# Optimization experiments

Hardware: AMD Instinct MI355X
Metric: run time of the kernel (lower is better)

Reference implementation:

```python
import jax, jax.numpy as jnp
import numpy as np

# Module dims (match init_kwargs)
D_IN = 1024
N_PRI = 2048
D_PRI = 16
N_CLS = 25
D_CLS = 16
ITERS = 3
B = 64
EPS = 1e-6


def layer_norm(x, g, b, eps=1e-5):
    m = x.mean(-1, keepdims=True)
    v = ((x - m) ** 2).mean(-1, keepdims=True)
    return (x - m) / jnp.sqrt(v + eps) * g + b


def setup_inputs() -> dict:
    key = jax.random.key(0)
    ks = jax.random.split(key, 6)
    s = lambda n: 1.0 / np.sqrt(n)
    return {
        "z": jax.random.normal(ks[0], (B, D_IN), jnp.float32),
        # to_primary: Linear(d_in, n_primary*d_primary)
        "w1": jax.random.normal(ks[1], (D_IN, N_PRI * D_PRI), jnp.float32) * s(D_IN),
        "b1": jnp.zeros((N_PRI * D_PRI,), jnp.float32),
        # primary_act: LayerNorm(d_in) -> Linear(d_in, n_primary) -> Sigmoid
        "ln1_g": jnp.ones((D_IN,), jnp.float32),
        "ln1_b": jnp.zeros((D_IN,), jnp.float32),
        "w2": jax.random.normal(ks[2], (D_IN, N_PRI), jnp.float32) * s(D_IN),
        "b2": jnp.zeros((N_PRI,), jnp.float32),
        # CapsuleFC transform + EM routing params
        "w_caps": jax.random.normal(ks[3], (N_PRI, D_PRI, N_CLS, D_CLS), jnp.float32) * s(D_PRI),
        "beta_u": jnp.zeros((N_CLS,), jnp.float32),
        "beta_a": jnp.zeros((N_CLS,), jnp.float32),
        # to_logits: LayerNorm(d_class) -> Linear(d_class, 1)
        "ln2_g": jnp.ones((D_CLS,), jnp.float32),
        "ln2_b": jnp.zeros((D_CLS,), jnp.float32),
        "w3": jax.random.normal(ks[4], (D_CLS, 1), jnp.float32) * s(D_CLS),
        "b3": jnp.zeros((1,), jnp.float32),
    }


def em_routing(V, a_in, beta_u, beta_a, n_iter):
    # V: (b, n_in, n_out, d) votes; a_in: (b, n_in) primary activations
    b, n, o, d = V.shape
    R = jnp.full((b, n, o), 1.0 / o, V.dtype)  # routing assignments
    lam = jnp.asarray(1.0, V.dtype)            # inverse temperature
    for _ in range(n_iter):
        # M-step: weighted mean/variance per output capsule
        r = R * a_in[:, :, None]                                  # (b,n,o)
        r_sum = r.sum(axis=1) + EPS                               # (b,o)
        mu = jnp.einsum('bno,bnod->bod', r, V) / r_sum[..., None]  # (b,o,d)
        diff2 = (V - mu[:, None]) ** 2                            # (b,n,o,d)
        sigma2 = jnp.einsum('bno,bnod->bod', r, diff2) / r_sum[..., None] + EPS
        cost = (beta_u[None, :, None] + 0.5 * jnp.log(sigma2)) * r_sum[..., None]
        a_out = jax.nn.sigmoid(lam * (beta_a[None, :] - cost.sum(-1)))  # (b,o)
        # E-step: Gaussian log-likelihood of each vote under each output capsule
        logp = (-0.5 * (diff2 / sigma2[:, None]).sum(-1)
                - 0.5 * jnp.log(sigma2).sum(-1)[:, None, :])      # (b,n,o)
        R = jax.nn.softmax(jnp.log(a_out + EPS)[:, None, :] + logp, axis=-1)
    return mu, a_out, R


def reference(z, w1, b1, ln1_g, ln1_b, w2, b2, w_caps, beta_u, beta_a,
              ln2_g, ln2_b, w3, b3):
    b = z.shape[0]
    # primary poses (no squash: use_squash_primary=False)
    primary_pose = (z @ w1 + b1).reshape(b, N_PRI, D_PRI)
    # primary activations
    primary_act = jnp.clip(jax.nn.sigmoid(layer_norm(z, ln1_g, ln1_b) @ w2 + b2), 0.0, 1.0)
    # votes: each primary capsule predicts each class capsule's pose
    V = jnp.einsum('bni,niod->bnod', primary_pose, w_caps)  # (B, N_PRI, N_CLS, D_CLS)
    class_pose, class_act, q = em_routing(V, primary_act, beta_u, beta_a, ITERS)
    logits = (layer_norm(class_pose, ln2_g, ln2_b) @ w3 + b3).squeeze(-1)  # (B, N_CLS)
    acts = jnp.linalg.norm(class_pose, axis=-1)                            # (B, N_CLS)
    return logits, acts, class_pose, q
```

## Files before the change

kernel.cpp:

```cpp
#include <hip/hip_runtime.h>
#include <hip/hip_bf16.h>
#include <cstdio>

#define B     64
#define DIN   1024
#define NPRI  2048
#define DPRI  16
#define NCLS  25
#define DCLS  16
#define EMEPS 1e-6f
#define LNEPS 1e-5f
#define KS2   8
#define NCH   32

#define OFF_POSE 0
#define OFF_ZN   (OFF_POSE + NPRI*DPRI*B)
#define OFF_ACTT (OFF_ZN + B*DIN)
#define OFF_G2P  (OFF_ACTT + NPRI*B)
#define OFF_V    (OFF_G2P + KS2*NPRI*B)
#define V_FLOATS (NPRI*NCLS*B*DCLS/2)
#define OFF_R    (OFF_V + V_FLOATS)
#define R_FLOATS (NPRI*NCLS*B/2)
#define OFF_PART (OFF_R + R_FLOATS)
#define OFF_MU   (OFF_PART + NCLS*NCH*33*B)
#define OFF_MI4  (OFF_MU + NCLS*DCLS*B)
#define OFF_BASE (OFF_MI4 + NCLS*8*B*4)
#define OFF_ZH   (OFF_BASE + NCLS*B)
#define WS_FLOATS (OFF_ZH + B*DIN/2)

typedef __attribute__((ext_vector_type(8))) _Float16 f16x8;
typedef __attribute__((ext_vector_type(4))) float f32x4;

__device__ __forceinline__ unsigned pack_f16(float a, float b) {
  union { _Float16 h[2]; unsigned u; } x;
  x.h[0] = (_Float16)a; x.h[1] = (_Float16)b;
  return x.u;
}
__device__ __forceinline__ float f16lo(unsigned u) {
  union { unsigned u; _Float16 h[2]; } x; x.u = u; return (float)x.h[0];
}
__device__ __forceinline__ float f16hi(unsigned u) {
  union { unsigned u; _Float16 h[2]; } x; x.u = u; return (float)x.h[1];
}
__device__ __forceinline__ unsigned short f16bits(float a) {
  union { _Float16 h; unsigned short u; } x; x.h = (_Float16)a; return x.u;
}
__device__ __forceinline__ float f16val(unsigned short u) {
  union { unsigned short u; _Float16 h; } x; x.u = u; return (float)x.h;
}

__global__ __launch_bounds__(256) void k_lnzh(const float* __restrict__ z,
                                              const float* __restrict__ g,
                                              const float* __restrict__ bb,
                                              float* __restrict__ zn,
                                              unsigned* __restrict__ zh) {
  int row = blockIdx.x, t = threadIdx.x;
  const float* zr = z + row * DIN;
  float4 v = ((const float4*)zr)[t];
  uint2 hz = {pack_f16(v.x, v.y), pack_f16(v.z, v.w)};
  *(uint2*)&zh[row * 512 + t * 2] = hz;
  float s  = v.x + v.y + v.z + v.w;
  float s2 = v.x*v.x + v.y*v.y + v.z*v.z + v.w*v.w;
  for (int off = 32; off; off >>= 1) {
    s  += __shfl_down(s, off);
    s2 += __shfl_down(s2, off);
  }
  __shared__ float ls[8];
  int wv = t >> 6, ln = t & 63;
  if (ln == 0) { ls[wv*2] = s; ls[wv*2+1] = s2; }
  __syncthreads();
  s  = ls[0] + ls[2] + ls[4] + ls[6];
  s2 = ls[1] + ls[3] + ls[5] + ls[7];
  float mean = s * (1.0f / DIN);
  float var  = s2 * (1.0f / DIN) - mean * mean;
  float inv  = 1.0f / sqrtf(var + LNEPS);
  float4 gg = ((const float4*)g)[t];
  float4 bv = ((const float4*)bb)[t];
  float4 o;
  o.x = (v.x - mean) * inv * gg.x + bv.x;
  o.y = (v.y - mean) * inv * gg.y + bv.y;
  o.z = (v.z - mean) * inv * gg.z + bv.z;
  o.w = (v.w - mean) * inv * gg.w + bv.w;
  ((float4*)(zn + row * DIN))[t] = o;
}

__global__ __launch_bounds__(512) void k_gemm1m(const unsigned* __restrict__ zh,
                                                const float* __restrict__ w1,
                                                const float* __restrict__ b1,
                                                float* __restrict__ poseT) {
  __shared__ __align__(16) unsigned bt[2][64 * 68];
  __shared__ __align__(16) unsigned zl[2][64 * 68];
  int t = threadIdx.x;
  int c0 = blockIdx.x * 64;
  int l = t & 63, w = t >> 6;
  int kh = w >> 2, cw = w & 3;
  int c15 = l & 15, kq = l >> 4;
  int h  = t >> 8;
  int th = t & 255;
  int s_kp = th >> 2;
  int s_q  = th & 3;

  f32x4 acc0 = {0,0,0,0}, acc1 = {0,0,0,0}, acc2 = {0,0,0,0}, acc3 = {0,0,0,0};

  float4 wr0[4], wr1[4];
  uint4  zr4[4];
  {
    int k0 = h * 512;
#pragma unroll
    for (int u = 0; u < 4; ++u) {
      int cq = s_q + 4 * u;
      const float* src0 = w1 + (size_t)(k0 + 2 * s_kp) * 32768 + c0 + cq * 4;
      wr0[u] = *(const float4*)src0;
      wr1[u] = *(const float4*)(src0 + 32768);
      zr4[u] = *(const uint4*)&zh[(size_t)s_kp * 512 + (k0 >> 1) + cq * 4];
    }
  }

  for (int it = 0; it < 4; ++it) {
#pragma unroll
    for (int u = 0; u < 4; ++u) {
      int cq = s_q + 4 * u;
      unsigned* dst = &bt[h][(cq * 4) * 68 + s_kp];
      dst[0]   = pack_f16(wr0[u].x, wr1[u].x);
      dst[68]  = pack_f16(wr0[u].y, wr1[u].y);
      dst[136] = pack_f16(wr0[u].z, wr1[u].z);
      dst[204] = pack_f16(wr0[u].w, wr1[u].w);
      *(uint4*)&zl[h][s_kp * 68 + cq * 4] = zr4[u];
    }
    __syncthreads();
    if (it < 3) {
      int k0n = (h * 4 + it + 1) * 128;
#pragma unroll
      for (int u = 0; u < 4; ++u) {
        int cq = s_q + 4 * u;
        const float* src0 = w1 + (size_t)(k0n + 2 * s_kp) * 32768 + c0 + cq * 4;
        wr0[u] = *(const float4*)src0;
        wr1[u] = *(const float4*)(src0 + 32768);
        zr4[u] = *(const uint4*)&zh[(size_t)s_kp * 512 + (k0n >> 1) + cq * 4];
      }
    }
#pragma unroll
    for (int ks = 0; ks < 4; ++ks) {
      union { uint4 u; f16x8 hh; } bf, a0, a1, a2, a3;
      bf.u = *(const uint4*)&bt[kh][(cw * 16 + c15) * 68 + ks * 16 + kq * 4];
      a0.u = *(const uint4*)&zl[kh][(c15)      * 68 + ks * 16 + kq * 4];
      a1.u = *(const uint4*)&zl[kh][(16 + c15) * 68 + ks * 16 + kq * 4];
      a2.u = *(const uint4*)&zl[kh][(32 + c15) * 68 + ks * 16 + kq * 4];
      a3.u = *(const uint4*)&zl[kh][(48 + c15) * 68 + ks * 16 + kq * 4];
      acc0 = __builtin_amdgcn_mfma_f32_16x16x32_f16(a0.hh, bf.hh, acc0, 0, 0, 0);
      acc1 = __builtin_amdgcn_mfma_f32_16x16x32_f16(a1.hh, bf.hh, acc1, 0, 0, 0);
      acc2 = __builtin_amdgcn_mfma_f32_16x16x32_f16(a2.hh, bf.hh, acc2, 0, 0, 0);
      acc3 = __builtin_amdgcn_mfma_f32_16x16x32_f16(a3.hh, bf.hh, acc3, 0, 0, 0);
    }
    __syncthreads();
  }

  float* red = (float*)&zl[0][0];
  if (kh == 1) {
    int cc = cw * 16 + c15;
    *(float4*)&red[cc * 68 + kq * 4]      = *(float4*)&acc0;
    *(float4*)&red[cc * 68 + 16 + kq * 4] = *(float4*)&acc1;
    *(float4*)&red[cc * 68 + 32 + kq * 4] = *(float4*)&acc2;
    *(float4*)&red[cc * 68 + 48 + kq * 4] = *(float4*)&acc3;
  }
  __syncthreads();
  if (kh == 0) {
    int cc = cw * 16 + c15;
    int c = c0 + cc;
    float bc = b1[c];
    float4 r0 = *(float4*)&red[cc * 68 + kq * 4];
    float4 r1 = *(float4*)&red[cc * 68 + 16 + kq * 4];
    float4 r2 = *(float4*)&red[cc * 68 + 32 + kq * 4];
    float4 r3 = *(float4*)&red[cc * 68 + 48 + kq * 4];
    float* pdst = poseT + (size_t)c * 64 + kq * 4;
    float4 o0 = {acc0[0] + r0.x + bc, acc0[1] + r0.y + bc, acc0[2] + r0.z + bc, acc0[3] + r0.w + bc};
    float4 o1 = {acc1[0] + r1.x + bc, acc1[1] + r1.y + bc, acc1[2] + r1.z + bc, acc1[3] + r1.w + bc};
    float4 o2 = {acc2[0] + r2.x + bc, acc2[1] + r2.y + bc, acc2[2] + r2.z + bc, acc2[3] + r2.w + bc};
    float4 o3 = {acc3[0] + r3.x + bc, acc3[1] + r3.y + bc, acc3[2] + r3.z + bc, acc3[3] + r3.w + bc};
    *(float4*)&pdst[0]  = o0;
    *(float4*)&pdst[16] = o1;
    *(float4*)&pdst[32] = o2;
    *(float4*)&pdst[48] = o3;
  }
}

__global__ __launch_bounds__(256, 2) void k_gemm2p(const float* __restrict__ zn,
                                                   const float* __restrict__ w2,
                                                   float* __restrict__ part) {
  __shared__ __align__(16) float znT[128 * 68];
  __shared__ __align__(16) float wl[128 * 68];
  int t = threadIdx.x;
  int c0 = blockIdx.x * 64;
  int k0 = blockIdx.y * 128;
  int zr_ = t >> 2, za = t & 3;
  int wk = t >> 1, wc = (t & 1) * 32;

#pragma unroll
  for (int jj = 0; jj < 4; ++jj) {
    int kb = za * 8 + jj * 32;
    const float* src = zn + zr_ * DIN + k0 + kb;
    float4 v0 = *(const float4*)src;
    float4 v1 = *(const float4*)(src + 4);
    znT[(kb+0)*68 + zr_] = v0.x; znT[(kb+1)*68 + zr_] = v0.y;
    znT[(kb+2)*68 + zr_] = v0.z; znT[(kb+3)*68 + zr_] = v0.w;
    znT[(kb+4)*68 + zr_] = v1.x; znT[(kb+5)*68 + zr_] = v1.y;
    znT[(kb+6)*68 + zr_] = v1.z; znT[(kb+7)*68 + zr_] = v1.w;
  }
  const float* wsrc = w2 + (size_t)(k0 + wk) * NPRI + c0 + wc;
#pragma unroll
  for (int j = 0; j < 8; ++j)
    *(float4*)&wl[wk * 68 + wc + j * 4] = *(const float4*)(wsrc + j * 4);
  __syncthreads();

  int r0 = (t >> 4) * 4, c0l = (t & 15) * 4;
  float acc[4][4];
#pragma unroll
  for (int j = 0; j < 4; ++j)
#pragma unroll
    for (int i = 0; i < 4; ++i) acc[j][i] = 0.f;

#pragma unroll 4
  for (int k = 0; k < 128; ++k) {
    float4 z4 = *(const float4*)&znT[k * 68 + r0];
    float4 w4 = *(const float4*)&wl[k * 68 + c0l];
    float zz[4] = {z4.x, z4.y, z4.z, z4.w};
    float ww[4] = {w4.x, w4.y, w4.z, w4.w};
#pragma unroll
    for (int j = 0; j < 4; ++j)
#pragma unroll
      for (int i = 0; i < 4; ++i) acc[j][i] += ww[j] * zz[i];
  }
  float* pdst = part + ((size_t)blockIdx.y * NPRI + c0 + c0l) * 64 + r0;
#pragma unroll
  for (int j = 0; j < 4; ++j) {
    float4 o = {acc[j][0], acc[j][1], acc[j][2], acc[j][3]};
    *(float4*)&pdst[j * 64] = o;
  }
}

__global__ __launch_bounds__(256) void k_gemm2r(const float* __restrict__ part,
                                                const float* __restrict__ b2,
                                                float* __restrict__ actt) {
  int idx = blockIdx.x * 256 + threadIdx.x;
  float4 s = {0.f, 0.f, 0.f, 0.f};
#pragma unroll
  for (int kz = 0; kz < KS2; ++kz) {
    float4 v = *(const float4*)&part[(size_t)kz * NPRI * 64 + idx * 4];
    s.x += v.x; s.y += v.y; s.z += v.z; s.w += v.w;
  }
  int c = (idx * 4) >> 6;
  float bc = b2[c];
  float4 o;
  o.x = fminf(fmaxf(1.0f / (1.0f + expf(-(s.x + bc))), 0.0f), 1.0f);
  o.y = fminf(fmaxf(1.0f / (1.0f + expf(-(s.y + bc))), 0.0f), 1.0f);
  o.z = fminf(fmaxf(1.0f / (1.0f + expf(-(s.z + bc))), 0.0f), 1.0f);
  o.w = fminf(fmaxf(1.0f / (1.0f + expf(-(s.w + bc))), 0.0f), 1.0f);
  *(float4*)&actt[idx * 4] = o;
}

__global__ __launch_bounds__(256) void k_votes(const float* __restrict__ poseT,
                                               const float* __restrict__ wcaps,
                                               unsigned* __restrict__ V) {
  __shared__ __align__(16) float wl[6400];
  __shared__ __align__(16) float pl[64 * 16];
  int n = blockIdx.x, t = threadIdx.x;
  const float* wsrc = wcaps + (size_t)n * 6400;
  for (int idx = t * 4; idx < 6400; idx += 1024)
    *(float4*)(wl + idx) = *(const float4*)(wsrc + idx);
  {
    float4 v = *(const float4*)(poseT + n * 1024 + t * 4);
    int i = (t * 4) >> 6, b = (t * 4) & 63;
    pl[(b+0)*16 + i] = v.x; pl[(b+1)*16 + i] = v.y;
    pl[(b+2)*16 + i] = v.z; pl[(b+3)*16 + i] = v.w;
  }
  __syncthreads();
  if (t >= 200) return;
  int o = t / 8, d0 = (t % 8) * 2;
  float w0[16], w1_[16];
#pragma unroll
  for (int i = 0; i < 16; ++i) {
    w0[i]  = wl[(i * 25 + o) * 16 + d0];
    w1_[i] = wl[(i * 25 + o) * 16 + d0 + 1];
  }
  unsigned* vd = V + (((size_t)n * 25 + o) * 64 * 16 + d0) / 2;
  for (int b = 0; b < 64; ++b) {
    const float* pb = &pl[b * 16];
    float a0 = 0.f, a1 = 0.f;
#pragma unroll
    for (int i = 0; i < 16; ++i) {
      float p = pb[i];
      a0 += p * w0[i];
      a1 += p * w1_[i];
    }
    vd[b * 8] = pack_f16(a0, a1);
  }
}

template <bool UNIFORM>
__global__ __launch_bounds__(256) void k_stats(const unsigned* __restrict__ V,
                                               const float* __restrict__ actt,
                                               const unsigned short* __restrict__ Rh,
                                               float* __restrict__ part) {
  int o = blockIdx.y;
  int t = threadIdx.x, b = t & 63, wv = t >> 6;
  float S0 = 0.f, S1[16], S2[16];
#pragma unroll
  for (int d = 0; d < 16; ++d) { S1[d] = 0.f; S2[d] = 0.f; }
  int n0 = blockIdx.x * 64 + wv * 16;
#pragma unroll 2
  for (int k = 0; k < 16; ++k) {
    int n = n0 + k;
    float a = actt[n * 64 + b];
    float r = UNIFORM ? a * (1.0f / 25.0f)
                      : f16val(Rh[((size_t)n * 25 + o) * 64 + b]) * a;
    const uint4* vp = (const uint4*)(V + (((size_t)n * 25 + o) * 64 + b) * 8);
    uint4 u0 = vp[0], u1 = vp[1];
    unsigned uu[8] = {u0.x, u0.y, u0.z, u0.w, u1.x, u1.y, u1.z, u1.w};
    S0 += r;
#pragma unroll
    for (int q = 0; q < 8; ++q) {
      float v0 = f16lo(uu[q]), v1 = f16hi(uu[q]);
      float t0 = r * v0, t1 = r * v1;
      S1[2*q]   += t0;          S1[2*q+1] += t1;
      S2[2*q]   += t0 * v0;     S2[2*q+1] += t1 * v1;
    }
  }
  __shared__ float red[4 * 33 * 64];
  red[(wv * 33 + 0) * 64 + b] = S0;
#pragma unroll
  for (int d = 0; d < 16; ++d) {
    red[(wv * 33 + 1 + d) * 64 + b]  = S1[d];
    red[(wv * 33 + 17 + d) * 64 + b] = S2[d];
  }
  __syncthreads();
  if (wv == 0) {
    for (int s = 0; s < 33; ++s) {
      float tot = red[s * 64 + b] + red[(33 + s) * 64 + b] +
                  red[(66 + s) * 64 + b] + red[(99 + s) * 64 + b];
      part[((o * NCH + blockIdx.x) * 33 + s) * 64 + b] = tot;
    }
  }
}

template <bool FINAL>
__global__ __launch_bounds__(256) void k_redfin(const float* __restrict__ part,
                                                const float* __restrict__ beta_u,
                                                const float* __restrict__ beta_a,
                                                float* __restrict__ mu,
                                                float* __restrict__ mi4,
                                                float* __restrict__ basew,
                                                const float* __restrict__ g2,
                                                const float* __restrict__ bb2,
                                                const float* __restrict__ w3,
                                                const float* __restrict__ b3,
                                                float* __restrict__ out) {
  __shared__ float st[33 * 64];
  int o = blockIdx.x, t = threadIdx.x;
  for (int slot = t; slot < 33 * 64; slot += 256) {
    float s = 0.f;
    const float* pp = part + (size_t)o * NCH * 2112 + slot;
    for (int c = 0; c < NCH; ++c) s += pp[(size_t)c * 2112];
    st[slot] = s;
  }
  __syncthreads();
  if (t < 64) {
    int b = t;
    float s0 = st[b];
    float rsm = s0 + EMEPS;
    float inv_rs = 1.0f / rsm;
    float ldet = 0.f;
    float mloc[16], iloc[16];
#pragma unroll
    for (int d = 0; d < 16; ++d) {
      float s1 = st[(1 + d) * 64 + b];
      float s2 = st[(17 + d) * 64 + b];
      float m = s1 * inv_rs;
      float var = (s2 - 2.0f * m * s1 + m * m * s0) * inv_rs;
      float sg = fmaxf(var, 0.0f) + EMEPS;
      mloc[d] = m;
      iloc[d] = 1.0f / sg;
      mu[(o * 16 + d) * 64 + b] = m;
      ldet += logf(sg);
    }
#pragma unroll
    for (int q = 0; q < 8; ++q) {
      float4 v = {mloc[2*q], iloc[2*q], mloc[2*q+1], iloc[2*q+1]};
      *(float4*)&mi4[((o * 8 + q) * 64 + b) * 4] = v;
    }
    float cost = (16.0f * beta_u[o] + 0.5f * ldet) * rsm;
    float x = beta_a[o] - cost;
    float a = 1.0f / (1.0f + expf(-x));
    basew[o * 64 + b] = logf(a + EMEPS) - 0.5f * ldet;

    if (FINAL) {
      float sm = 0.f;
#pragma unroll
      for (int d = 0; d < 16; ++d) sm += mloc[d];
      float mean = sm * (1.0f / 16.0f);
      float var2 = 0.f;
#pragma unroll
      for (int d = 0; d < 16; ++d) { float dd = mloc[d] - mean; var2 += dd * dd; }
      var2 *= (1.0f / 16.0f);
      float inv2 = 1.0f / sqrtf(var2 + LNEPS);
      float logit = 0.f, nrm = 0.f;
#pragma unroll
      for (int d = 0; d < 16; ++d) {
        float nh = (mloc[d] - mean) * inv2 * g2[d] + bb2[d];
        logit += nh * w3[d];
        nrm += mloc[d] * mloc[d];
      }
      out[b * 25 + o] = logit + b3[0];
      out[1600 + b * 25 + o] = sqrtf(nrm);
      float* pp = out + 3200 + (b * 25 + o) * 16;
#pragma unroll
      for (int d = 0; d < 16; ++d) pp[d] = mloc[d];
    }
  }
}

template <bool FINAL>
__global__ __launch_bounds__(256) void k_estep(const unsigned* __restrict__ V,
                                               const float* __restrict__ mi4,
                                               const float* __restrict__ basew,
                                               unsigned short* __restrict__ Rh,
                                               float* __restrict__ qout) {
  int t = threadIdx.x, b = t & 63, ng = t >> 6;
  int n = blockIdx.x * 4 + ng;
  float l[25];
  float mx = -1e30f;
#pragma unroll
  for (int o = 0; o < 25; ++o) {
    const uint4* vp = (const uint4*)(V + (((size_t)n * 25 + o) * 64 + b) * 8);
    uint4 u0 = vp[0], u1 = vp[1];
    unsigned uu[8] = {u0.x, u0.y, u0.z, u0.w, u1.x, u1.y, u1.z, u1.w};
    float acc = 0.f;
#pragma unroll
    for (int qq = 0; qq < 8; ++qq) {
      float4 mi = *(const float4*)&mi4[((o * 8 + qq) * 64 + b) * 4];
      float d0 = f16lo(uu[qq]) - mi.x;
      float d1 = f16hi(uu[qq]) - mi.z;
      acc += d0 * d0 * mi.y + d1 * d1 * mi.w;
    }
    l[o] = basew[o * 64 + b] - 0.5f * acc;
    mx = fmaxf(mx, l[o]);
  }
  float s = 0.f;
#pragma unroll
  for (int o = 0; o < 25; ++o) { l[o] = expf(l[o] - mx); s += l[o]; }
  float inv = 1.0f / s;
  if (FINAL) {
    float* qp = qout + ((size_t)b * NPRI + n) * 25;
#pragma unroll
    for (int o = 0; o < 25; ++o) qp[o] = l[o] * inv;
  } else {
#pragma unroll
    for (int o = 0; o < 25; ++o)
      Rh[((size_t)n * 25 + o) * 64 + b] = f16bits(l[o] * inv);
  }
}

extern "C" void kernel_launch(void* const* d_in, const int* in_sizes, int n_in,
                              void* d_out, int out_size, void* d_ws, size_t ws_size,
                              hipStream_t stream) {
  const float* z      = (const float*)d_in[0];
  const float* w1     = (const float*)d_in[1];
  const float* b1     = (const float*)d_in[2];
  const float* ln1g   = (const float*)d_in[3];
  const float* ln1b   = (const float*)d_in[4];
  const float* w2     = (const float*)d_in[5];
  const float* b2     = (const float*)d_in[6];
  const float* wcaps  = (const float*)d_in[7];
  const float* beta_u = (const float*)d_in[8];
  const float* beta_a = (const float*)d_in[9];
  const float* ln2g   = (const float*)d_in[10];
  const float* ln2b   = (const float*)d_in[11];
  const float* w3     = (const float*)d_in[12];
  const float* b3     = (const float*)d_in[13];

  if (ws_size < (size_t)WS_FLOATS * 4) {
    fprintf(stderr, "kernel_launch: ws too small: %zu < %zu bytes\n",
            ws_size, (size_t)WS_FLOATS * 4);
  }

  float* ws    = (float*)d_ws;
  float* out   = (float*)d_out;
  float* poseT = ws + OFF_POSE;
  float* zn    = ws + OFF_ZN;
  float* actt  = ws + OFF_ACTT;
  float* g2p   = ws + OFF_G2P;
  unsigned* V  = (unsigned*)(ws + OFF_V);
  unsigned short* Rh = (unsigned short*)(ws + OFF_R);
  float* part  = ws + OFF_PART;
  float* muw   = ws + OFF_MU;
  float* mi4   = ws + OFF_MI4;
  float* bse   = ws + OFF_BASE;
  unsigned* zh = (unsigned*)(ws + OFF_ZH);

  k_lnzh<<<64, 256, 0, stream>>>(z, ln1g, ln1b, zn, zh);
  k_gemm1m<<<512, 512, 0, stream>>>(zh, w1, b1, poseT);
  k_gemm2p<<<dim3(32, KS2), 256, 0, stream>>>(zn, w2, g2p);
  k_gemm2r<<<128, 256, 0, stream>>>(g2p, b2, actt);
  k_votes<<<2048, 256, 0, stream>>>(poseT, wcaps, V);

  k_stats<true><<<dim3(NCH, 25), 256, 0, stream>>>(V, actt, Rh, part);
  k_redfin<false><<<25, 256, 0, stream>>>(part, beta_u, beta_a, muw, mi4, bse,
                                          ln2g, ln2b, w3, b3, out);

  k_estep<false><<<512, 256, 0, stream>>>(V, mi4, bse, Rh, nullptr);
  k_stats<false><<<dim3(NCH, 25), 256, 0, stream>>>(V, actt, Rh, part);
  k_redfin<false><<<25, 256, 0, stream>>>(part, beta_u, beta_a, muw, mi4, bse,
                                          ln2g, ln2b, w3, b3, out);

  k_estep<false><<<512, 256, 0, stream>>>(V, mi4, bse, Rh, nullptr);
  k_stats<false><<<dim3(NCH, 25), 256, 0, stream>>>(V, actt, Rh, part);
  k_redfin<true><<<25, 256, 0, stream>>>(part, beta_u, beta_a, muw, mi4, bse,
                                         ln2g, ln2b, w3, b3, out);

  k_estep<true><<<512, 256, 0, stream>>>(V, mi4, bse, nullptr, out + 28800);
}
```

Baseline: 381.2 us.

## Drop GEMM1 register prefetch, halve stats chunks, remove unused mu writes

```diff
diff --git a/kernel.cpp b/kernel.cpp
--- a/kernel.cpp
+++ b/kernel.cpp
@@ -11,7 +11,7 @@
 #define EMEPS 1e-6f
 #define LNEPS 1e-5f
 #define KS2   8
-#define NCH   32
+#define NCH   16
 
 #define OFF_POSE 0
 #define OFF_ZN   (OFF_POSE + NPRI*DPRI*B)
@@ -102,43 +102,27 @@
 
   f32x4 acc0 = {0,0,0,0}, acc1 = {0,0,0,0}, acc2 = {0,0,0,0}, acc3 = {0,0,0,0};
 
-  float4 wr0[4], wr1[4];
-  uint4  zr4[4];
-  {
-    int k0 = h * 512;
+  for (int it = 0; it < 4; ++it) {
+    int k0 = (h * 4 + it) * 128;
 #pragma unroll
     for (int u = 0; u < 4; ++u) {
       int cq = s_q + 4 * u;
       const float* src0 = w1 + (size_t)(k0 + 2 * s_kp) * 32768 + c0 + cq * 4;
-      wr0[u] = *(const float4*)src0;
-      wr1[u] = *(const float4*)(src0 + 32768);
-      zr4[u] = *(const uint4*)&zh[(size_t)s_kp * 512 + (k0 >> 1) + cq * 4];
-    }
-  }
-
-  for (int it = 0; it < 4; ++it) {
+      float4 r0 = *(const float4*)src0;
+      float4 r1 = *(const float4*)(src0 + 32768);
+      unsigned* dst = &bt[h][(cq * 4) * 68 + s_kp];
+      dst[0]   = pack_f16(r0.x, r1.x);
+      dst[68]  = pack_f16(r0.y, r1.y);
+      dst[136] = pack_f16(r0.z, r1.z);
+      dst[204] = pack_f16(r0.w, r1.w);
+    }
 #pragma unroll
     for (int u = 0; u < 4; ++u) {
-      int cq = s_q + 4 * u;
-      unsigned* dst = &bt[h][(cq * 4) * 68 + s_kp];
-      dst[0]   = pack_f16(wr0[u].x, wr1[u].x);
-      dst[68]  = pack_f16(wr0[u].y, wr1[u].y);
-      dst[136] = pack_f16(wr0[u].z, wr1[u].z);
-      dst[204] = pack_f16(wr0[u].w, wr1[u].w);
-      *(uint4*)&zl[h][s_kp * 68 + cq * 4] = zr4[u];
+      int ku4 = s_q + 4 * u;
+      uint4 v = *(const uint4*)&zh[(size_t)s_kp * 512 + (k0 >> 1) + ku4 * 4];
+      *(uint4*)&zl[h][s_kp * 68 + ku4 * 4] = v;
     }
     __syncthreads();
-    if (it < 3) {
-      int k0n = (h * 4 + it + 1) * 128;
-#pragma unroll
-      for (int u = 0; u < 4; ++u) {
-        int cq = s_q + 4 * u;
-        const float* src0 = w1 + (size_t)(k0n + 2 * s_kp) * 32768 + c0 + cq * 4;
-        wr0[u] = *(const float4*)src0;
-        wr1[u] = *(const float4*)(src0 + 32768);
-        zr4[u] = *(const uint4*)&zh[(size_t)s_kp * 512 + (k0n >> 1) + cq * 4];
-      }
-    }
 #pragma unroll
     for (int ks = 0; ks < 4; ++ks) {
       union { uint4 u; f16x8 hh; } bf, a0, a1, a2, a3;
@@ -306,9 +290,8 @@
   float S0 = 0.f, S1[16], S2[16];
 #pragma unroll
   for (int d = 0; d < 16; ++d) { S1[d] = 0.f; S2[d] = 0.f; }
-  int n0 = blockIdx.x * 64 + wv * 16;
-#pragma unroll 2
-  for (int k = 0; k < 16; ++k) {
+  int n0 = blockIdx.x * 128 + wv * 32;
+  for (int k = 0; k < 32; ++k) {
     int n = n0 + k;
     float a = actt[n * 64 + b];
     float r = UNIFORM ? a * (1.0f / 25.0f)
@@ -346,7 +329,6 @@
 __global__ __launch_bounds__(256) void k_redfin(const float* __restrict__ part,
                                                 const float* __restrict__ beta_u,
                                                 const float* __restrict__ beta_a,
-                                                float* __restrict__ mu,
                                                 float* __restrict__ mi4,
                                                 float* __restrict__ basew,
                                                 const float* __restrict__ g2,
@@ -359,6 +341,7 @@
   for (int slot = t; slot < 33 * 64; slot += 256) {
     float s = 0.f;
     const float* pp = part + (size_t)o * NCH * 2112 + slot;
+#pragma unroll
     for (int c = 0; c < NCH; ++c) s += pp[(size_t)c * 2112];
     st[slot] = s;
   }
@@ -379,7 +362,6 @@
       float sg = fmaxf(var, 0.0f) + EMEPS;
       mloc[d] = m;
       iloc[d] = 1.0f / sg;
-      mu[(o * 16 + d) * 64 + b] = m;
       ldet += logf(sg);
     }
 #pragma unroll
@@ -491,7 +473,6 @@
   unsigned* V  = (unsigned*)(ws + OFF_V);
   unsigned short* Rh = (unsigned short*)(ws + OFF_R);
   float* part  = ws + OFF_PART;
-  float* muw   = ws + OFF_MU;
   float* mi4   = ws + OFF_MI4;
   float* bse   = ws + OFF_BASE;
   unsigned* zh = (unsigned*)(ws + OFF_ZH);
@@ -503,17 +484,17 @@
   k_votes<<<2048, 256, 0, stream>>>(poseT, wcaps, V);
 
   k_stats<true><<<dim3(NCH, 25), 256, 0, stream>>>(V, actt, Rh, part);
-  k_redfin<false><<<25, 256, 0, stream>>>(part, beta_u, beta_a, muw, mi4, bse,
+  k_redfin<false><<<25, 256, 0, stream>>>(part, beta_u, beta_a, mi4, bse,
                                           ln2g, ln2b, w3, b3, out);
 
   k_estep<false><<<512, 256, 0, stream>>>(V, mi4, bse, Rh, nullptr);
   k_stats<false><<<dim3(NCH, 25), 256, 0, stream>>>(V, actt, Rh, part);
-  k_redfin<false><<<25, 256, 0, stream>>>(part, beta_u, beta_a, muw, mi4, bse,
+  k_redfin<false><<<25, 256, 0, stream>>>(part, beta_u, beta_a, mi4, bse,
                                           ln2g, ln2b, w3, b3, out);
 
   k_estep<false><<<512, 256, 0, stream>>>(V, mi4, bse, Rh, nullptr);
   k_stats<false><<<dim3(NCH, 25), 256, 0, stream>>>(V, actt, Rh, part);
-  k_redfin<true><<<25, 256, 0, stream>>>(part, beta_u, beta_a, muw, mi4, bse,
+  k_redfin<true><<<25, 256, 0, stream>>>(part, beta_u, beta_a, mi4, bse,
                                          ln2g, ln2b, w3, b3, out);
 
   k_estep<true><<<512, 256, 0, stream>>>(V, mi4, bse, nullptr, out + 28800);
```

Measured after the change: 350.0 us. 1.09x faster.
